# Optimization experiments

Hardware: AMD Instinct MI355X
Metric: run time of the kernel (lower is better)

The kernel has to match this reference:

```python
import jax, jax.numpy as jnp
import numpy as np

D_MODEL, D_K, D_V = 1024, 64, 64

def setup_inputs() -> dict:
    key = jax.random.key(0)
    ks = jax.random.split(key, 7)
    s = 1.0 / np.sqrt(D_MODEL)
    return {
        "x": jax.random.normal(ks[0], (4, 4096, D_MODEL), dtype=jnp.float32),
        "w_q": jax.random.normal(ks[1], (D_MODEL, D_K), dtype=jnp.float32) * s,
        "b_q": jnp.zeros((D_K,), dtype=jnp.float32),
        "w_k": jax.random.normal(ks[2], (D_MODEL, D_K), dtype=jnp.float32) * s,
        "b_k": jnp.zeros((D_K,), dtype=jnp.float32),
        "w_v": jax.random.normal(ks[3], (D_MODEL, D_V), dtype=jnp.float32) * s,
        "b_v": jnp.zeros((D_V,), dtype=jnp.float32),
    }

def reference(x, w_q, b_q, w_k, b_k, w_v, b_v):
    # x: [b, s, d_model]
    q = x @ w_q + b_q                      # [b, s, d_k]
    k = x @ w_k + b_k                      # [b, s, d_k]
    v = x @ w_v + b_v                      # [b, s, d_v]
    scores = jnp.einsum("bqd,bkd->bqk", q, k) / jnp.sqrt(jnp.float32(D_K))
    seq_len = scores.shape[-1]
    causal = jnp.tril(jnp.ones((seq_len, seq_len), dtype=bool))  # keep lower-tri
    scores = jnp.where(causal, scores, -jnp.inf)
    probs = jax.nn.softmax(scores, axis=-1)
    return jnp.einsum("bqk,bkd->bqd", probs, v)  # [b, s, d_v]
```

## Files before the change

kernel.cpp:

```cpp
#include <hip/hip_runtime.h>
#include <hip/hip_bf16.h>

using f32x4    = __attribute__((ext_vector_type(4))) float;
using f32x16   = __attribute__((ext_vector_type(16))) float;
using bf16x8   = __attribute__((ext_vector_type(8))) __bf16;
using ushort8  = __attribute__((ext_vector_type(8))) unsigned short;
using ushort4v = __attribute__((ext_vector_type(4))) unsigned short;
using uint4v   = __attribute__((ext_vector_type(4))) unsigned int;
using float4v  = __attribute__((ext_vector_type(4))) float;

#define LOG2E 1.44269504088896340736f
#define SHIFT_L2 5.77078016355585f

static __device__ __forceinline__ unsigned short f2bf(float f) {
  union { __hip_bfloat16 h; unsigned short u; } cv;
  cv.h = __float2bfloat16(f);
  return cv.u;
}
static __device__ __forceinline__ bf16x8 ld_bf8_g(const void* p) {
  ushort8 u = *(const ushort8*)p;
  return __builtin_bit_cast(bf16x8, u);
}
static __device__ __forceinline__ float fast_exp2(float x) {
#if __has_builtin(__builtin_amdgcn_exp2f)
  return __builtin_amdgcn_exp2f(x);
#else
  return exp2f(x);
#endif
}
static __device__ __forceinline__ unsigned int pk2(float a, float b) {
  return (unsigned int)f2bf(a) | ((unsigned int)f2bf(b) << 16);
}

__global__ __launch_bounds__(256) void wprep_kernel(
    const float* __restrict__ wq, const float* __restrict__ wk,
    const float* __restrict__ wv, unsigned short* __restrict__ Wfrag) {
  int idx = blockIdx.x * 256 + threadIdx.x;
  int col = idx >> 10;
  int k   = idx & 1023;
  const float* w = (col < 64) ? wq : (col < 128) ? wk : wv;
  int c = col & 63;
  int n = col >> 4, l15 = col & 15;
  int kk = k >> 5, lh = (k >> 3) & 3, e = k & 7;
  size_t elem = ((size_t)(n * 32 + kk) * 64 + lh * 16 + l15) * 8 + e;
  Wfrag[elem] = f2bf(w[k * 64 + c]);
}

__global__ __launch_bounds__(256, 2) void proj_kernel(
    const float* __restrict__ x, const unsigned short* __restrict__ Wfrag,
    const float* __restrict__ bq, const float* __restrict__ bk,
    const float* __restrict__ bv,
    unsigned short* __restrict__ qb, unsigned short* __restrict__ kreg,
    unsigned short* __restrict__ vreg) {
  __shared__ __align__(16) char As[2][32 * 128];
  int tid = threadIdx.x, wave = tid >> 6, lane = tid & 63;
  int rowBase = blockIdx.x * 32;
  int rhalf = (wave & 1) * 16;
  int nbase = (wave >> 1) * 6;
  int l15 = lane & 15, lh = lane >> 4;

  int arow = tid >> 3, ac0 = (tid & 7) * 8;
  const float* xp = x + (size_t)(rowBase + arow) * 1024 + ac0;
  int abyte = (arow * 128 + ac0 * 2) ^ ((arow & 7) << 4);
  const char* wfb = (const char*)Wfrag + (size_t)lane * 16;

  f32x4 acc[6];
#pragma unroll
  for (int i = 0; i < 6; ++i) acc[i] = (f32x4){0.f, 0.f, 0.f, 0.f};

  float4v aL[3], aH[3];
  bf16x8 B[2][12];

  {
    float4v t0 = *(const float4v*)(xp);
    float4v t1 = *(const float4v*)(xp + 4);
#pragma unroll
    for (int j = 0; j < 6; ++j) {
      B[0][j * 2]     = ld_bf8_g(wfb + (((size_t)(nbase + j) * 32 + 0) << 10));
      B[0][j * 2 + 1] = ld_bf8_g(wfb + (((size_t)(nbase + j) * 32 + 1) << 10));
    }
    ushort8 u;
#pragma unroll
    for (int e = 0; e < 4; ++e) { u[e] = f2bf(t0[e]); u[4 + e] = f2bf(t1[e]); }
    *(ushort8*)(As[0] + abyte) = u;
  }
#pragma unroll
  for (int d = 1; d <= 3; ++d) {
    aL[d % 3] = *(const float4v*)(xp + d * 64);
    aH[d % 3] = *(const float4v*)(xp + d * 64 + 4);
  }
  asm volatile("s_waitcnt lgkmcnt(0)" ::: "memory");
  __builtin_amdgcn_s_barrier();
  __builtin_amdgcn_sched_barrier(0);

#pragma unroll
  for (int kt = 0; kt < 16; ++kt) {
    const int cur = kt & 1, nxt = cur ^ 1;
    if (kt < 15) {
#pragma unroll
      for (int j = 0; j < 6; ++j) {
        B[nxt][j * 2]     = ld_bf8_g(wfb + (((size_t)(nbase + j) * 32 + 2 * (kt + 1)) << 10));
        B[nxt][j * 2 + 1] = ld_bf8_g(wfb + (((size_t)(nbase + j) * 32 + 2 * (kt + 1) + 1) << 10));
      }
    }
    {
      int row = rhalf + l15;
      bf16x8 a0 = ld_bf8_g(As[cur] + ((row * 128 + lh * 16) ^ ((row & 7) << 4)));
      bf16x8 a1 = ld_bf8_g(As[cur] + ((row * 128 + 64 + lh * 16) ^ ((row & 7) << 4)));
#pragma unroll
      for (int j = 0; j < 6; ++j) {
        acc[j] = __builtin_amdgcn_mfma_f32_16x16x32_bf16(a0, B[cur][j * 2], acc[j], 0, 0, 0);
        acc[j] = __builtin_amdgcn_mfma_f32_16x16x32_bf16(a1, B[cur][j * 2 + 1], acc[j], 0, 0, 0);
      }
    }
    if (kt < 15) {
      const int s = (kt + 1) % 3;
      ushort8 u;
#pragma unroll
      for (int e = 0; e < 4; ++e) { u[e] = f2bf(aL[s][e]); u[4 + e] = f2bf(aH[s][e]); }
      *(ushort8*)(As[nxt] + abyte) = u;
      if (kt + 4 < 16) {
        aL[s] = *(const float4v*)(xp + (kt + 4) * 64);
        aH[s] = *(const float4v*)(xp + (kt + 4) * 64 + 4);
      }
      asm volatile("s_waitcnt lgkmcnt(0)" ::: "memory");
      __builtin_amdgcn_s_barrier();
      __builtin_amdgcn_sched_barrier(0);
    }
  }

#pragma unroll
  for (int cf = 0; cf < 6; ++cf) {
    int col = (nbase + cf) * 16 + l15;
    int sel = col >> 6, c64 = col & 63;
    const float* bias = (sel == 0) ? bq : (sel == 1) ? bk : bv;
    float bb = bias[c64];
    if (sel == 0) {
#pragma unroll
      for (int r = 0; r < 4; ++r) {
        int row = rowBase + rhalf + lh * 4 + r;
        qb[(size_t)row * 64 + c64] = f2bf((acc[cf][r] + bb) * (0.125f * LOG2E));
      }
    } else if (sel == 1) {
      int j16 = c64 >> 4, hik = (c64 >> 3) & 1, e = c64 & 7;
#pragma unroll
      for (int r = 0; r < 4; ++r) {
        int s = rowBase + rhalf + lh * 4 + r;
        int b = s >> 12, sl = s & 4095;
        int ch = sl >> 7, kvw = sl & 127;
        int kvq = kvw >> 5, lk = kvw & 31;
        size_t off = (((size_t)(b * 32 + ch)) << 14) + kvq * 4096 + j16 * 1024 +
                     (hik * 32 + lk) * 16 + e * 2;
        *(unsigned short*)((char*)kreg + off) = f2bf(acc[cf][r] + bb);
      }
    } else {
      ushort4v w;
#pragma unroll
      for (int r = 0; r < 4; ++r) w[r] = f2bf(acc[cf][r] + bb);
      int s0 = rowBase + rhalf + lh * 4;
      int b = s0 >> 12, sl = s0 & 4095;
      int ch = sl >> 7, kvw = sl & 127;
      int kvq = kvw >> 5, k5 = kvw & 31;
      int kj = k5 >> 4, hiv = (k5 >> 3) & 1, e0 = k5 & 7;
      int dt = c64 >> 5, lv = c64 & 31, f = kj * 2 + dt;
      size_t off = (((size_t)(b * 32 + ch)) << 14) + kvq * 4096 + f * 1024 +
                   (hiv * 32 + lv) * 16 + e0 * 2;
      *(ushort4v*)((char*)vreg + off) = w;
    }
  }
}

__global__ __launch_bounds__(64, 4) void attn_kernel(
    const unsigned short* __restrict__ qb, const unsigned short* __restrict__ kreg,
    const unsigned short* __restrict__ vreg, float* __restrict__ po,
    float* __restrict__ lo) {
  int lane = threadIdx.x & 63;
  int l31 = lane & 31, hi = lane >> 5;
  int wid = blockIdx.x;
  int T = 127 - (wid >> 5);
  int low = wid & 31;
  int batch = low & 3, ph = low >> 2;
  int Tq = T * 32;
  const size_t bO = (size_t)batch * 262144;
  const char* kb = (const char*)kreg + ((size_t)batch << 19);
  const char* vb = (const char*)vreg + ((size_t)batch << 19);

  const unsigned short* qp = qb + bO + (size_t)(Tq + l31) * 64 + hi * 8;
  bf16x8 qf0 = ld_bf8_g(qp);
  bf16x8 qf1 = ld_bf8_g(qp + 16);
  bf16x8 qf2 = ld_bf8_g(qp + 32);
  bf16x8 qf3 = ld_bf8_g(qp + 48);

  f32x16 o0, o1;
#pragma unroll
  for (int r = 0; r < 16; ++r) { o0[r] = 0.f; o1[r] = 0.f; }
  float lsum = 0.f;

#pragma unroll 1
  for (int st = ph; st <= T; st += 8) {
    size_t base = ((size_t)(st >> 2) << 14) + (st & 3) * 4096 + lane * 16;
    const char* kp = kb + base;
    const char* vp = vb + base;
    bf16x8 k0 = ld_bf8_g(kp);
    bf16x8 k1 = ld_bf8_g(kp + 1024);
    bf16x8 k2 = ld_bf8_g(kp + 2048);
    bf16x8 k3 = ld_bf8_g(kp + 3072);
    bf16x8 v0 = ld_bf8_g(vp);
    bf16x8 v1 = ld_bf8_g(vp + 1024);
    bf16x8 v2 = ld_bf8_g(vp + 2048);
    bf16x8 v3 = ld_bf8_g(vp + 3072);

    f32x16 sc;
#pragma unroll
    for (int r = 0; r < 16; ++r) sc[r] = 0.f;
    sc = __builtin_amdgcn_mfma_f32_32x32x16_bf16(k0, qf0, sc, 0, 0, 0);
    sc = __builtin_amdgcn_mfma_f32_32x32x16_bf16(k1, qf1, sc, 0, 0, 0);
    sc = __builtin_amdgcn_mfma_f32_32x32x16_bf16(k2, qf2, sc, 0, 0, 0);
    sc = __builtin_amdgcn_mfma_f32_32x32x16_bf16(k3, qf3, sc, 0, 0, 0);
    if (st == T) {
      int qg = Tq + l31;
#pragma unroll
      for (int r = 0; r < 16; ++r) {
        int kvg = 32 * st + (r & 3) + 8 * (r >> 2) + 4 * hi;
        if (kvg > qg) sc[r] = -3.0e38f;
      }
    }
    float pv[16];
#pragma unroll
    for (int r = 0; r < 16; ++r) {
      pv[r] = fast_exp2(sc[r] - SHIFT_L2);
      lsum += pv[r];
    }
#pragma unroll
    for (int kj = 0; kj < 2; ++kj) {
      const int R = 8 * kj;
      unsigned int A0 = pk2(pv[R + 0], pv[R + 1]);
      unsigned int A1 = pk2(pv[R + 2], pv[R + 3]);
      unsigned int B0 = pk2(pv[R + 4], pv[R + 5]);
      unsigned int B1 = pk2(pv[R + 6], pv[R + 7]);
      unsigned int s0 = hi ? A0 : B0;
      unsigned int s1 = hi ? A1 : B1;
      unsigned int r0 = __shfl_xor((int)s0, 32, 64);
      unsigned int r1 = __shfl_xor((int)s1, 32, 64);
      uint4v dw = {hi ? r0 : A0, hi ? r1 : A1, hi ? B0 : r0, hi ? B1 : r1};
      bf16x8 pa = __builtin_bit_cast(bf16x8, dw);
      if (kj == 0) {
        o0 = __builtin_amdgcn_mfma_f32_32x32x16_bf16(pa, v0, o0, 0, 0, 0);
        o1 = __builtin_amdgcn_mfma_f32_32x32x16_bf16(pa, v1, o1, 0, 0, 0);
      } else {
        o0 = __builtin_amdgcn_mfma_f32_32x32x16_bf16(pa, v2, o0, 0, 0, 0);
        o1 = __builtin_amdgcn_mfma_f32_32x32x16_bf16(pa, v3, o1, 0, 0, 0);
      }
    }
  }

  lsum += __shfl_xor(lsum, 32, 64);

  float* pdst = po + (size_t)ph * 1048576 + bO + (size_t)Tq * 64;
#pragma unroll
  for (int r = 0; r < 16; ++r) {
    int qloc = (r & 3) + 8 * (r >> 2) + 4 * hi;
    pdst[qloc * 64 + l31] = o0[r];
    pdst[qloc * 64 + 32 + l31] = o1[r];
  }
  if (hi == 0) lo[ph * 16384 + batch * 4096 + Tq + l31] = lsum;
}

__global__ __launch_bounds__(256) void merge_kernel(
    const float* __restrict__ po, const float* __restrict__ lo,
    float* __restrict__ out) {
  int i = blockIdx.x * 256 + threadIdx.x;
  int row = i >> 4;
  float4v a = ((const float4v*)po)[i];
  float L = lo[row];
#pragma unroll
  for (int ph = 1; ph < 8; ++ph) {
    a += ((const float4v*)po)[i + ph * 262144];
    L += lo[row + ph * 16384];
  }
  a *= (1.0f / L);
  ((float4v*)out)[i] = a;
}

extern "C" void kernel_launch(void* const* d_in, const int* in_sizes, int n_in,
                              void* d_out, int out_size, void* d_ws, size_t ws_size,
                              hipStream_t stream) {
  const float* x  = (const float*)d_in[0];
  const float* wq = (const float*)d_in[1];
  const float* bq = (const float*)d_in[2];
  const float* wk = (const float*)d_in[3];
  const float* bk = (const float*)d_in[4];
  const float* wv = (const float*)d_in[5];
  const float* bv = (const float*)d_in[6];

  unsigned short* Wfrag = (unsigned short*)d_ws;
  unsigned short* qbuf  = Wfrag + 192 * 1024;
  unsigned short* kreg  = qbuf + 16384 * 64;
  unsigned short* vreg  = kreg + 16384 * 64;
  float*          po    = (float*)(vreg + 16384 * 64);
  float*          lo    = po + 8 * 1048576;

  wprep_kernel<<<768, 256, 0, stream>>>(wq, wk, wv, Wfrag);
  proj_kernel<<<512, 256, 0, stream>>>(x, Wfrag, bq, bk, bv, qbuf, kreg, vreg);
  attn_kernel<<<4096, 64, 0, stream>>>(qbuf, kreg, vreg, po, lo);
  merge_kernel<<<1024, 256, 0, stream>>>(po, lo, (float*)d_out);
}
```

Baseline: 56.46 us.

## Double the projection K-tile to 128 to halve barrier count

```diff
diff --git a/kernel.cpp b/kernel.cpp
--- a/kernel.cpp
+++ b/kernel.cpp
@@ -52,76 +52,90 @@
     const float* __restrict__ bv,
     unsigned short* __restrict__ qb, unsigned short* __restrict__ kreg,
     unsigned short* __restrict__ vreg) {
-  __shared__ __align__(16) char As[2][32 * 128];
+  __shared__ __align__(16) char As[2][32 * 256];
   int tid = threadIdx.x, wave = tid >> 6, lane = tid & 63;
   int rowBase = blockIdx.x * 32;
   int rhalf = (wave & 1) * 16;
   int nbase = (wave >> 1) * 6;
   int l15 = lane & 15, lh = lane >> 4;
 
-  int arow = tid >> 3, ac0 = (tid & 7) * 8;
-  const float* xp = x + (size_t)(rowBase + arow) * 1024 + ac0;
-  int abyte = (arow * 128 + ac0 * 2) ^ ((arow & 7) << 4);
+  int arow = tid >> 3, ac8 = (tid & 7);
+  const float* xp = x + (size_t)(rowBase + arow) * 1024 + ac8 * 16;
+  int abyte = (arow * 256 + ac8 * 32) ^ ((arow & 7) << 4);
   const char* wfb = (const char*)Wfrag + (size_t)lane * 16;
 
   f32x4 acc[6];
 #pragma unroll
   for (int i = 0; i < 6; ++i) acc[i] = (f32x4){0.f, 0.f, 0.f, 0.f};
 
-  float4v aL[3], aH[3];
+  float4v aR[2][4];
   bf16x8 B[2][12];
 
   {
     float4v t0 = *(const float4v*)(xp);
     float4v t1 = *(const float4v*)(xp + 4);
+    float4v t2 = *(const float4v*)(xp + 8);
+    float4v t3 = *(const float4v*)(xp + 12);
 #pragma unroll
     for (int j = 0; j < 6; ++j) {
       B[0][j * 2]     = ld_bf8_g(wfb + (((size_t)(nbase + j) * 32 + 0) << 10));
       B[0][j * 2 + 1] = ld_bf8_g(wfb + (((size_t)(nbase + j) * 32 + 1) << 10));
     }
-    ushort8 u;
-#pragma unroll
-    for (int e = 0; e < 4; ++e) { u[e] = f2bf(t0[e]); u[4 + e] = f2bf(t1[e]); }
-    *(ushort8*)(As[0] + abyte) = u;
-  }
-#pragma unroll
-  for (int d = 1; d <= 3; ++d) {
-    aL[d % 3] = *(const float4v*)(xp + d * 64);
-    aH[d % 3] = *(const float4v*)(xp + d * 64 + 4);
-  }
+    ushort8 u0, u1;
+#pragma unroll
+    for (int e = 0; e < 4; ++e) {
+      u0[e] = f2bf(t0[e]); u0[4 + e] = f2bf(t1[e]);
+      u1[e] = f2bf(t2[e]); u1[4 + e] = f2bf(t3[e]);
+    }
+    *(ushort8*)(As[0] + abyte) = u0;
+    *(ushort8*)(As[0] + (abyte ^ 16)) = u1;
+  }
+#pragma unroll
+  for (int d = 1; d <= 2; ++d)
+#pragma unroll
+    for (int q4 = 0; q4 < 4; ++q4)
+      aR[d & 1][q4] = *(const float4v*)(xp + d * 128 + q4 * 4);
   asm volatile("s_waitcnt lgkmcnt(0)" ::: "memory");
   __builtin_amdgcn_s_barrier();
   __builtin_amdgcn_sched_barrier(0);
 
 #pragma unroll
-  for (int kt = 0; kt < 16; ++kt) {
-    const int cur = kt & 1, nxt = cur ^ 1;
-    if (kt < 15) {
+  for (int kt2 = 0; kt2 < 8; ++kt2) {
+    const int cur = kt2 & 1, nxt = cur ^ 1;
+#pragma unroll
+    for (int cp = 0; cp < 2; ++cp) {
+      const int kkp = kt2 * 2 + cp;
+      const int bc = kkp & 1, bn = bc ^ 1;
+      if (kkp + 1 < 16) {
+#pragma unroll
+        for (int j = 0; j < 6; ++j) {
+          B[bn][j * 2]     = ld_bf8_g(wfb + (((size_t)(nbase + j) * 32 + 2 * (kkp + 1)) << 10));
+          B[bn][j * 2 + 1] = ld_bf8_g(wfb + (((size_t)(nbase + j) * 32 + 2 * (kkp + 1) + 1) << 10));
+        }
+      }
+      int row = rhalf + l15;
+      bf16x8 a0 = ld_bf8_g(As[cur] + ((row * 256 + cp * 128 + lh * 16) ^ ((row & 7) << 4)));
+      bf16x8 a1 = ld_bf8_g(As[cur] + ((row * 256 + cp * 128 + 64 + lh * 16) ^ ((row & 7) << 4)));
 #pragma unroll
       for (int j = 0; j < 6; ++j) {
-        B[nxt][j * 2]     = ld_bf8_g(wfb + (((size_t)(nbase + j) * 32 + 2 * (kt + 1)) << 10));
-        B[nxt][j * 2 + 1] = ld_bf8_g(wfb + (((size_t)(nbase + j) * 32 + 2 * (kt + 1) + 1) << 10));
-      }
-    }
-    {
-      int row = rhalf + l15;
-      bf16x8 a0 = ld_bf8_g(As[cur] + ((row * 128 + lh * 16) ^ ((row & 7) << 4)));
-      bf16x8 a1 = ld_bf8_g(As[cur] + ((row * 128 + 64 + lh * 16) ^ ((row & 7) << 4)));
-#pragma unroll
-      for (int j = 0; j < 6; ++j) {
-        acc[j] = __builtin_amdgcn_mfma_f32_16x16x32_bf16(a0, B[cur][j * 2], acc[j], 0, 0, 0);
-        acc[j] = __builtin_amdgcn_mfma_f32_16x16x32_bf16(a1, B[cur][j * 2 + 1], acc[j], 0, 0, 0);
-      }
-    }
-    if (kt < 15) {
-      const int s = (kt + 1) % 3;
-      ushort8 u;
-#pragma unroll
-      for (int e = 0; e < 4; ++e) { u[e] = f2bf(aL[s][e]); u[4 + e] = f2bf(aH[s][e]); }
-      *(ushort8*)(As[nxt] + abyte) = u;
-      if (kt + 4 < 16) {
-        aL[s] = *(const float4v*)(xp + (kt + 4) * 64);
-        aH[s] = *(const float4v*)(xp + (kt + 4) * 64 + 4);
+        acc[j] = __builtin_amdgcn_mfma_f32_16x16x32_bf16(a0, B[bc][j * 2], acc[j], 0, 0, 0);
+        acc[j] = __builtin_amdgcn_mfma_f32_16x16x32_bf16(a1, B[bc][j * 2 + 1], acc[j], 0, 0, 0);
+      }
+    }
+    if (kt2 < 7) {
+      const int s = (kt2 + 1) & 1;
+      ushort8 u0, u1;
+#pragma unroll
+      for (int e = 0; e < 4; ++e) {
+        u0[e] = f2bf(aR[s][0][e]); u0[4 + e] = f2bf(aR[s][1][e]);
+        u1[e] = f2bf(aR[s][2][e]); u1[4 + e] = f2bf(aR[s][3][e]);
+      }
+      *(ushort8*)(As[nxt] + abyte) = u0;
+      *(ushort8*)(As[nxt] + (abyte ^ 16)) = u1;
+      if (kt2 + 3 < 8) {
+#pragma unroll
+        for (int q4 = 0; q4 < 4; ++q4)
+          aR[s][q4] = *(const float4v*)(xp + (kt2 + 3) * 128 + q4 * 4);
       }
       asm volatile("s_waitcnt lgkmcnt(0)" ::: "memory");
       __builtin_amdgcn_s_barrier();
```

Result: no change. 57.51 us (+1.9%).
